# Performance work log

Hardware: AMD Instinct MI355X
Metric: run time of the kernel (lower is better)

The kernel has to match this reference:

```python
import jax, jax.numpy as jnp
import numpy as np

NUM_HEADS = 8

def setup_inputs() -> dict:
    key = jax.random.key(0)
    ks = jax.random.split(key, 10)
    B, S, D = 4, 2048, 512
    scale = 1.0 / np.sqrt(D)
    return {
        "x": jax.random.normal(ks[0], (B, S, D), dtype=jnp.float32),
        "q": jax.random.normal(ks[1], (B, S, D), dtype=jnp.float32),
        "Wq": jax.random.normal(ks[2], (D, D), dtype=jnp.float32) * scale,
        "bq": jax.random.normal(ks[3], (D,), dtype=jnp.float32) * 0.01,
        "Wk": jax.random.normal(ks[4], (D, D), dtype=jnp.float32) * scale,
        "bk": jax.random.normal(ks[5], (D,), dtype=jnp.float32) * 0.01,
        "Wv": jax.random.normal(ks[6], (D, D), dtype=jnp.float32) * scale,
        "bv": jax.random.normal(ks[7], (D,), dtype=jnp.float32) * 0.01,
        "Wo": jax.random.normal(ks[8], (D, D), dtype=jnp.float32) * scale,
        "bo": jax.random.normal(ks[9], (D,), dtype=jnp.float32) * 0.01,
    }

def reference(x, q, Wq, bq, Wk, bk, Wv, bv, Wo, bo):
    B, S, D = x.shape
    H = NUM_HEADS
    Dh = D // H
    # Linear layers: y = x @ W.T + b (torch nn.Linear convention)
    def split_heads(t):  # [B,S,D] -> [B,H,S,Dh]
        return t.reshape(B, -1, H, Dh).transpose(0, 2, 1, 3)
    Q = split_heads(q @ Wq.T + bq)
    K = split_heads(x @ Wk.T + bk)
    V = split_heads(x @ Wv.T + bv)
    logits = jnp.einsum('bhqd,bhkd->bhqk', Q, K) / jnp.sqrt(jnp.asarray(Dh, Q.dtype))
    attn = jax.nn.softmax(logits, axis=-1)
    out = jnp.einsum('bhqk,bhkd->bhqd', attn, V)  # [B,H,S,Dh]
    concat = out.transpose(0, 2, 1, 3).reshape(B, -1, D)
    return concat @ Wo.T + bo
```

## Files before the change

kernel.cpp:

```cpp
#include <hip/hip_runtime.h>
#include <stdint.h>

typedef __bf16 bf16_t;
typedef bf16_t bf16x8 __attribute__((ext_vector_type(8)));
typedef bf16_t bf16x4 __attribute__((ext_vector_type(4)));
typedef bf16_t bf16x2 __attribute__((ext_vector_type(2)));
typedef float f32x4 __attribute__((ext_vector_type(4)));
typedef float f32x16 __attribute__((ext_vector_type(16)));
typedef uint32_t u32x4 __attribute__((ext_vector_type(4)));

#define DEV __device__ __forceinline__

DEV void gload_lds16(const void* g, void* l) {
  __builtin_amdgcn_global_load_lds(
      (__attribute__((address_space(1))) void*)(g),
      (__attribute__((address_space(3))) void*)(l), 16, 0, 0);
}

__global__ __launch_bounds__(256) void cvt2_kernel(
    const float* __restrict__ x, const float* __restrict__ q,
    bf16_t* __restrict__ xb, bf16_t* __restrict__ qb) {
  const float* s = blockIdx.y ? q : x;
  bf16_t* d = blockIdx.y ? qb : xb;
  int i = blockIdx.x * 256 + threadIdx.x;
  if (i < 524288) {
    const float4* sp = (const float4*)s + (size_t)i * 2;
    float4 a = sp[0], b = sp[1];
    bf16x8 o;
    o[0] = (bf16_t)a.x; o[1] = (bf16_t)a.y; o[2] = (bf16_t)a.z; o[3] = (bf16_t)a.w;
    o[4] = (bf16_t)b.x; o[5] = (bf16_t)b.y; o[6] = (bf16_t)b.z; o[7] = (bf16_t)b.w;
    *(bf16x8*)(d + (size_t)i * 8) = o;
  }
}

__global__ __launch_bounds__(256) void cvtw_kernel(
    const float* __restrict__ Wq, const float* __restrict__ Wk,
    const float* __restrict__ Wv, const float* __restrict__ Wo,
    bf16_t* __restrict__ dst) {
  int y = blockIdx.y;
  const float* s = (y == 0) ? Wq : (y == 1) ? Wk : (y == 2) ? Wv : Wo;
  bf16_t* d = dst + (size_t)y * 262144;
  int i = blockIdx.x * 256 + threadIdx.x;
  if (i < 32768) {
    const float4* sp = (const float4*)s + (size_t)i * 2;
    float4 a = sp[0], b = sp[1];
    bf16x8 o;
    o[0] = (bf16_t)a.x; o[1] = (bf16_t)a.y; o[2] = (bf16_t)a.z; o[3] = (bf16_t)a.w;
    o[4] = (bf16_t)b.x; o[5] = (bf16_t)b.y; o[6] = (bf16_t)b.z; o[7] = (bf16_t)b.w;
    *(bf16x8*)(d + (size_t)i * 8) = o;
  }
}

DEV void gemm_core(const bf16_t* __restrict__ A, const bf16_t* __restrict__ W,
                   char* smem, f32x4 (&acc)[4][4]) {
  const int tid = threadIdx.x;
  const int lane = tid & 63;
  const int wid = tid >> 6;
  const int wr = wid >> 1, wc = wid & 1;
  const int bx = blockIdx.x, by = blockIdx.y;

  uint32_t goffA[4], goffB[4], ldsoff[4];
#pragma unroll
  for (int c = 0; c < 4; ++c) {
    uint32_t o = (uint32_t)wid * 4096u + (uint32_t)c * 1024u + (uint32_t)lane * 16u;
    uint32_t row = o >> 7;
    uint32_t inner = (o & 127u) ^ ((row & 7u) << 4);
    goffA[c] = ((uint32_t)by * 128u + row) * 1024u + inner;
    goffB[c] = ((uint32_t)bx * 128u + row) * 1024u + inner;
    ldsoff[c] = o - (uint32_t)lane * 16u;
  }
  uint32_t offA[4][2], offB[4][2];
#pragma unroll
  for (int i = 0; i < 4; ++i)
#pragma unroll
    for (int kk = 0; kk < 2; ++kk) {
      uint32_t ra = (uint32_t)(wr * 64 + i * 16 + (lane & 15));
      offA[i][kk] = ra * 128u + (((uint32_t)kk * 64u + ((lane >> 4) * 16u)) ^ ((ra & 7u) << 4));
      uint32_t rb = (uint32_t)(wc * 64 + i * 16 + (lane & 15));
      offB[i][kk] = rb * 128u + (((uint32_t)kk * 64u + ((lane >> 4) * 16u)) ^ ((rb & 7u) << 4));
    }

  const char* Ab = (const char*)A;
  const char* Wb = (const char*)W;

#pragma unroll
  for (int c = 0; c < 4; ++c) {
    gload_lds16(Ab + goffA[c], smem + ldsoff[c]);
    gload_lds16(Wb + goffB[c], smem + 16384 + ldsoff[c]);
  }
  asm volatile("s_waitcnt vmcnt(0)" ::: "memory");
  __syncthreads();

#pragma unroll 1
  for (int kt = 0; kt < 8; ++kt) {
    const int buf = kt & 1;
    char* cur = smem + buf * 32768;
    if (kt < 7) {
      char* nxt = smem + (buf ^ 1) * 32768;
      uint32_t gk = (uint32_t)(kt + 1) * 128u;
#pragma unroll
      for (int c = 0; c < 4; ++c) {
        gload_lds16(Ab + goffA[c] + gk, nxt + ldsoff[c]);
        gload_lds16(Wb + goffB[c] + gk, nxt + 16384 + ldsoff[c]);
      }
    }
    bf16x8 af[4][2], bfr[4][2];
#pragma unroll
    for (int kk = 0; kk < 2; ++kk)
#pragma unroll
      for (int i = 0; i < 4; ++i) {
        af[i][kk] = *(const bf16x8*)(cur + offA[i][kk]);
        bfr[i][kk] = *(const bf16x8*)(cur + 16384 + offB[i][kk]);
      }
    __builtin_amdgcn_s_setprio(1);
#pragma unroll
    for (int kk = 0; kk < 2; ++kk)
#pragma unroll
      for (int mi = 0; mi < 4; ++mi)
#pragma unroll
        for (int nj = 0; nj < 4; ++nj)
          acc[mi][nj] = __builtin_amdgcn_mfma_f32_16x16x32_bf16(
              af[mi][kk], bfr[nj][kk], acc[mi][nj], 0, 0, 0);
    __builtin_amdgcn_s_setprio(0);
    asm volatile("s_waitcnt vmcnt(0)" ::: "memory");
    __syncthreads();
  }
}

__global__ __launch_bounds__(256) void gemm_qkv_kernel(
    const bf16_t* __restrict__ xb, const bf16_t* __restrict__ qb,
    const bf16_t* __restrict__ Wb, const float* __restrict__ bq,
    const float* __restrict__ bk, const float* __restrict__ bv,
    bf16_t* __restrict__ Qh, bf16_t* __restrict__ Kh, bf16_t* __restrict__ VT) {
  __shared__ char smem[65536];
  const int z = blockIdx.z;
  const bf16_t* A = (z == 0) ? qb : xb;
  const bf16_t* W = Wb + (size_t)z * 262144;
  const float* bias = (z == 0) ? bq : (z == 1) ? bk : bv;

  f32x4 acc[4][4] = {};
  gemm_core(A, W, smem, acc);

  const int lane = threadIdx.x & 63, wid = threadIdx.x >> 6;
  const int wr = wid >> 1, wc = wid & 1;
  const int colbase = blockIdx.x * 128 + wc * 64 + (lane & 15);
  const int rowbase = blockIdx.y * 128 + wr * 64 + ((lane >> 4) << 2);

  if (z == 2) {
#pragma unroll
    for (int nj = 0; nj < 4; ++nj) {
      int c = colbase + nj * 16;
      float bb = bias[c];
      int h = c >> 6, d = c & 63;
#pragma unroll
      for (int mi = 0; mi < 4; ++mi) {
        int r0 = rowbase + mi * 16;
        int b = r0 >> 11, s0 = r0 & 2047;
        bf16x4 v;
#pragma unroll
        for (int rr = 0; rr < 4; ++rr) v[rr] = (bf16_t)(acc[mi][nj][rr] + bb);
        *(bf16x4*)(VT + ((size_t)((b << 3) | h) * 64 + d) * 2048 + s0) = v;
      }
    }
  } else {
    bf16_t* O = (z == 0) ? Qh : Kh;
    const float scl = (z == 0) ? 0.18033688f : 1.0f;
#pragma unroll
    for (int nj = 0; nj < 4; ++nj) {
      int c = colbase + nj * 16;
      float bb = bias[c];
      int h = c >> 6, d = c & 63;
#pragma unroll
      for (int mi = 0; mi < 4; ++mi)
#pragma unroll
        for (int rr = 0; rr < 4; ++rr) {
          int r = rowbase + mi * 16 + rr;
          int b = r >> 11, s = r & 2047;
          O[((size_t)((b << 3) | h) * 2048 + s) * 64 + d] = (bf16_t)((acc[mi][nj][rr] + bb) * scl);
        }
    }
  }
}

__global__ __launch_bounds__(256) void gemm_out_kernel(
    const bf16_t* __restrict__ ctx, const bf16_t* __restrict__ Wo,
    const float* __restrict__ bo, float* __restrict__ out) {
  __shared__ char smem[65536];
  f32x4 acc[4][4] = {};
  gemm_core(ctx, Wo, smem, acc);

  const int lane = threadIdx.x & 63, wid = threadIdx.x >> 6;
  const int wr = wid >> 1, wc = wid & 1;
  const int colbase = blockIdx.x * 128 + wc * 64 + (lane & 15);
  const int rowbase = blockIdx.y * 128 + wr * 64 + ((lane >> 4) << 2);
#pragma unroll
  for (int nj = 0; nj < 4; ++nj) {
    int c = colbase + nj * 16;
    float bb = bo[c];
#pragma unroll
    for (int mi = 0; mi < 4; ++mi)
#pragma unroll
      for (int rr = 0; rr < 4; ++rr) {
        int r = rowbase + mi * 16 + rr;
        out[(size_t)r * 512 + c] = acc[mi][nj][rr] + bb;
      }
  }
}

__global__ __launch_bounds__(256, 2) void attn_kernel(
    const bf16_t* __restrict__ Qh, const bf16_t* __restrict__ Kh,
    const bf16_t* __restrict__ VT, bf16_t* __restrict__ ctx) {
  __shared__ char smem[32768];
  char* Kb = smem;
  char* Vb = smem + 16384;
  const int tid = threadIdx.x, lane = tid & 63, wid = tid >> 6;
  const int l31 = lane & 31, h = lane >> 5;
  const int qt = blockIdx.x, bh = blockIdx.y;

  const char* Kbase = (const char*)Kh + (size_t)bh * 262144;
  const char* Vbase = (const char*)VT + (size_t)bh * 262144;
  const char* Qbase = (const char*)Qh + (size_t)bh * 262144;

  const int qrow = qt * 128 + wid * 32 + l31;
  bf16x8 qf[4];
#pragma unroll
  for (int ks = 0; ks < 4; ++ks)
    qf[ks] = *(const bf16x8*)(Qbase + (size_t)qrow * 128 + ks * 32 + h * 16);

  uint32_t kgo[2], vgo[2], lo[2];
#pragma unroll
  for (int c = 0; c < 2; ++c) {
    uint32_t o = (uint32_t)c * 4096u + (uint32_t)wid * 1024u + (uint32_t)lane * 16u;
    uint32_t row = o >> 7;
    uint32_t inner = (o & 127u) ^ ((row & 7u) << 4);
    kgo[c] = row * 128u + inner;
    vgo[c] = row * 4096u + inner;
    lo[c] = o - (uint32_t)lane * 16u;
  }

  const uint32_t swz = (uint32_t)(l31 & 7) << 4;
  uint32_t fbase[2], fcol[4];
#pragma unroll
  for (int c = 0; c < 2; ++c) fbase[c] = (uint32_t)(32 * c + l31) * 128u;
#pragma unroll
  for (int ks = 0; ks < 4; ++ks) fcol[ks] = ((uint32_t)(ks * 32 + h * 16)) ^ swz;

  f32x16 oacc[2] = {};
  float m_run = -1.0e30f, l_part = 0.f;

#pragma unroll
  for (int c = 0; c < 2; ++c) {
    gload_lds16(Kbase + kgo[c], Kb + lo[c]);
    gload_lds16(Vbase + vgo[c], Vb + lo[c]);
  }
  asm volatile("s_waitcnt vmcnt(0)" ::: "memory");
  __syncthreads();

#pragma unroll 1
  for (int t = 0; t < 32; ++t) {
    const uint32_t cur = ((uint32_t)t & 1u) << 13;
    if (t < 31) {
      const uint32_t nxt = cur ^ 8192u;
      const char* Kn = Kbase + (size_t)(t + 1) * 8192;
      const char* Vn = Vbase + (size_t)(t + 1) * 128;
#pragma unroll
      for (int c = 0; c < 2; ++c) {
        gload_lds16(Kn + kgo[c], Kb + nxt + lo[c]);
        gload_lds16(Vn + vgo[c], Vb + nxt + lo[c]);
      }
    }

    f32x16 sT[2] = {};
#pragma unroll
    for (int c = 0; c < 2; ++c) {
      __builtin_amdgcn_s_setprio(1);
#pragma unroll
      for (int ks = 0; ks < 4; ++ks) {
        bf16x8 kf = *(const bf16x8*)(Kb + cur + fbase[c] + fcol[ks]);
        sT[c] = __builtin_amdgcn_mfma_f32_32x32x16_bf16(kf, qf[ks], sT[c], 0, 0, 0);
      }
      __builtin_amdgcn_s_setprio(0);
    }

    float mx = sT[0][0];
#pragma unroll
    for (int c = 0; c < 2; ++c)
#pragma unroll
      for (int r = 0; r < 16; ++r) mx = fmaxf(mx, sT[c][r]);
    mx = fmaxf(mx, __shfl_xor(mx, 32));
    bool ok = (mx <= m_run + 8.0f);
    if (!__all(ok)) {
      float mnew = fmaxf(m_run, mx);
      float sc = __builtin_exp2f(m_run - mnew);
      m_run = mnew;
      l_part *= sc;
#pragma unroll
      for (int r = 0; r < 16; ++r) { oacc[0][r] *= sc; oacc[1][r] *= sc; }
    }

    uint32_t cw[2][8];
    float ladd = 0.f;
#pragma unroll
    for (int c = 0; c < 2; ++c)
#pragma unroll
      for (int w = 0; w < 8; ++w) {
        float p0 = __builtin_exp2f(sT[c][2 * w] - m_run);
        float p1 = __builtin_exp2f(sT[c][2 * w + 1] - m_run);
        ladd += p0 + p1;
        bf16x2 tp; tp[0] = (bf16_t)p0; tp[1] = (bf16_t)p1;
        cw[c][w] = __builtin_bit_cast(uint32_t, tp);
      }
    l_part += ladd;

    bf16x8 pa[4];
#pragma unroll
    for (int s = 0; s < 4; ++s) {
      const int c = s >> 1, sp = s & 1;
      uint32_t w0 = cw[c][4 * sp + 0], w1 = cw[c][4 * sp + 1];
      uint32_t w2 = cw[c][4 * sp + 2], w3 = cw[c][4 * sp + 3];
      uint32_t sx0 = (uint32_t)__shfl_xor((int)w0, 32);
      uint32_t sx1 = (uint32_t)__shfl_xor((int)w1, 32);
      uint32_t sx2 = (uint32_t)__shfl_xor((int)w2, 32);
      uint32_t sx3 = (uint32_t)__shfl_xor((int)w3, 32);
      u32x4 ta;
      ta[0] = h ? sx2 : w0;
      ta[1] = h ? sx3 : w1;
      ta[2] = h ? w2 : sx0;
      ta[3] = h ? w3 : sx1;
      pa[s] = __builtin_bit_cast(bf16x8, ta);
    }

#pragma unroll
    for (int dc = 0; dc < 2; ++dc) {
      __builtin_amdgcn_s_setprio(1);
#pragma unroll
      for (int ks = 0; ks < 4; ++ks) {
        bf16x8 vf = *(const bf16x8*)(Vb + cur + fbase[dc] + fcol[ks]);
        oacc[dc] = __builtin_amdgcn_mfma_f32_32x32x16_bf16(vf, pa[ks], oacc[dc], 0, 0, 0);
      }
      __builtin_amdgcn_s_setprio(0);
    }

    asm volatile("s_waitcnt vmcnt(0)" ::: "memory");
    __syncthreads();
  }

  float l = l_part + __shfl_xor(l_part, 32);
  float inv = 1.0f / l;
  const int b = bh >> 3, hh = bh & 7;
  bf16_t* crow = ctx + ((size_t)(b * 2048 + qrow)) * 512 + hh * 64;
#pragma unroll
  for (int dc = 0; dc < 2; ++dc)
#pragma unroll
    for (int m = 0; m < 4; ++m) {
      bf16x4 v;
#pragma unroll
      for (int r = 0; r < 4; ++r) v[r] = (bf16_t)(oacc[dc][4 * m + r] * inv);
      *(bf16x4*)(crow + dc * 32 + m * 8 + h * 4) = v;
    }
}

extern "C" void kernel_launch(void* const* d_in, const int* in_sizes, int n_in,
                              void* d_out, int out_size, void* d_ws, size_t ws_size,
                              hipStream_t stream) {
  const float* x  = (const float*)d_in[0];
  const float* q  = (const float*)d_in[1];
  const float* Wq = (const float*)d_in[2];
  const float* bq = (const float*)d_in[3];
  const float* Wk = (const float*)d_in[4];
  const float* bk = (const float*)d_in[5];
  const float* Wv = (const float*)d_in[6];
  const float* bv = (const float*)d_in[7];
  const float* Wo = (const float*)d_in[8];
  const float* bo = (const float*)d_in[9];

  char* ws = (char*)d_ws;
  bf16_t* xb  = (bf16_t*)(ws + 0);
  bf16_t* qb  = (bf16_t*)(ws + 8388608);
  bf16_t* Wb  = (bf16_t*)(ws + 16777216);
  bf16_t* Qh  = (bf16_t*)(ws + 18874368);
  bf16_t* Kh  = (bf16_t*)(ws + 27262976);
  bf16_t* VT  = (bf16_t*)(ws + 35651584);
  bf16_t* ctx = (bf16_t*)(ws + 44040192);

  cvt2_kernel<<<dim3(2048, 2), 256, 0, stream>>>(x, q, xb, qb);
  cvtw_kernel<<<dim3(128, 4), 256, 0, stream>>>(Wq, Wk, Wv, Wo, Wb);
  gemm_qkv_kernel<<<dim3(4, 64, 3), 256, 0, stream>>>(xb, qb, Wb, bq, bk, bv, Qh, Kh, VT);
  attn_kernel<<<dim3(16, 32), 256, 0, stream>>>(Qh, Kh, VT, ctx);
  gemm_out_kernel<<<dim3(4, 64), 256, 0, stream>>>(ctx, Wb + 3 * 262144, bo, (float*)d_out);
}
```

Measured before the change: 121.2 us.

## Speculative softmax max, fused convert kernels, remapped attention blocks, fewer shuffles

```diff
diff --git a/kernel.cpp b/kernel.cpp
--- a/kernel.cpp
+++ b/kernel.cpp
@@ -17,38 +17,30 @@
       (__attribute__((address_space(3))) void*)(l), 16, 0, 0);
 }
 
-__global__ __launch_bounds__(256) void cvt2_kernel(
+__global__ __launch_bounds__(256) void cvt_all_kernel(
     const float* __restrict__ x, const float* __restrict__ q,
-    bf16_t* __restrict__ xb, bf16_t* __restrict__ qb) {
-  const float* s = blockIdx.y ? q : x;
-  bf16_t* d = blockIdx.y ? qb : xb;
-  int i = blockIdx.x * 256 + threadIdx.x;
-  if (i < 524288) {
-    const float4* sp = (const float4*)s + (size_t)i * 2;
-    float4 a = sp[0], b = sp[1];
-    bf16x8 o;
-    o[0] = (bf16_t)a.x; o[1] = (bf16_t)a.y; o[2] = (bf16_t)a.z; o[3] = (bf16_t)a.w;
-    o[4] = (bf16_t)b.x; o[5] = (bf16_t)b.y; o[6] = (bf16_t)b.z; o[7] = (bf16_t)b.w;
-    *(bf16x8*)(d + (size_t)i * 8) = o;
-  }
-}
-
-__global__ __launch_bounds__(256) void cvtw_kernel(
     const float* __restrict__ Wq, const float* __restrict__ Wk,
     const float* __restrict__ Wv, const float* __restrict__ Wo,
-    bf16_t* __restrict__ dst) {
-  int y = blockIdx.y;
-  const float* s = (y == 0) ? Wq : (y == 1) ? Wk : (y == 2) ? Wv : Wo;
-  bf16_t* d = dst + (size_t)y * 262144;
+    bf16_t* __restrict__ xb, bf16_t* __restrict__ qb, bf16_t* __restrict__ Wb) {
+  const int y = blockIdx.y;
   int i = blockIdx.x * 256 + threadIdx.x;
-  if (i < 32768) {
-    const float4* sp = (const float4*)s + (size_t)i * 2;
-    float4 a = sp[0], b = sp[1];
-    bf16x8 o;
-    o[0] = (bf16_t)a.x; o[1] = (bf16_t)a.y; o[2] = (bf16_t)a.z; o[3] = (bf16_t)a.w;
-    o[4] = (bf16_t)b.x; o[5] = (bf16_t)b.y; o[6] = (bf16_t)b.z; o[7] = (bf16_t)b.w;
-    *(bf16x8*)(d + (size_t)i * 8) = o;
-  }
+  const float* s;
+  bf16_t* d;
+  if (y == 0) { s = x; d = xb; }
+  else if (y == 1) { s = q; d = qb; }
+  else {
+    if (i >= 131072) return;
+    int widx = i >> 15;
+    s = (widx == 0) ? Wq : (widx == 1) ? Wk : (widx == 2) ? Wv : Wo;
+    d = Wb + (size_t)widx * 262144;
+    i &= 32767;
+  }
+  const float4* sp = (const float4*)s + (size_t)i * 2;
+  float4 a = sp[0], b = sp[1];
+  bf16x8 o;
+  o[0] = (bf16_t)a.x; o[1] = (bf16_t)a.y; o[2] = (bf16_t)a.z; o[3] = (bf16_t)a.w;
+  o[4] = (bf16_t)b.x; o[5] = (bf16_t)b.y; o[6] = (bf16_t)b.z; o[7] = (bf16_t)b.w;
+  *(bf16x8*)(d + (size_t)i * 8) = o;
 }
 
 DEV void gemm_core(const bf16_t* __restrict__ A, const bf16_t* __restrict__ W,
@@ -215,7 +207,9 @@
   char* Vb = smem + 16384;
   const int tid = threadIdx.x, lane = tid & 63, wid = tid >> 6;
   const int l31 = lane & 31, h = lane >> 5;
-  const int qt = blockIdx.x, bh = blockIdx.y;
+  const int bid = blockIdx.x + 16 * blockIdx.y;
+  const int qt = (bid >> 3) & 15;
+  const int bh = (bid & 7) * 4 + (bid >> 7);
 
   const char* Kbase = (const char*)Kh + (size_t)bh * 262144;
   const char* Vbase = (const char*)VT + (size_t)bh * 262144;
@@ -246,7 +240,7 @@
   for (int ks = 0; ks < 4; ++ks) fcol[ks] = ((uint32_t)(ks * 32 + h * 16)) ^ swz;
 
   f32x16 oacc[2] = {};
-  float m_run = -1.0e30f, l_part = 0.f;
+  float m_run = 0.0f, l_part = 0.f;
 
 #pragma unroll
   for (int c = 0; c < 2; ++c) {
@@ -282,34 +276,51 @@
       __builtin_amdgcn_s_setprio(0);
     }
 
-    float mx = sT[0][0];
-#pragma unroll
-    for (int c = 0; c < 2; ++c)
-#pragma unroll
-      for (int r = 0; r < 16; ++r) mx = fmaxf(mx, sT[c][r]);
-    mx = fmaxf(mx, __shfl_xor(mx, 32));
-    bool ok = (mx <= m_run + 8.0f);
-    if (!__all(ok)) {
-      float mnew = fmaxf(m_run, mx);
-      float sc = __builtin_exp2f(m_run - mnew);
-      m_run = mnew;
-      l_part *= sc;
-#pragma unroll
-      for (int r = 0; r < 16; ++r) { oacc[0][r] *= sc; oacc[1][r] *= sc; }
-    }
-
     uint32_t cw[2][8];
-    float ladd = 0.f;
+    float la0 = 0.f, la1 = 0.f, la2 = 0.f, la3 = 0.f;
 #pragma unroll
     for (int c = 0; c < 2; ++c)
 #pragma unroll
       for (int w = 0; w < 8; ++w) {
         float p0 = __builtin_exp2f(sT[c][2 * w] - m_run);
         float p1 = __builtin_exp2f(sT[c][2 * w + 1] - m_run);
-        ladd += p0 + p1;
+        if ((w & 3) == 0) la0 += p0 + p1;
+        else if ((w & 3) == 1) la1 += p0 + p1;
+        else if ((w & 3) == 2) la2 += p0 + p1;
+        else la3 += p0 + p1;
         bf16x2 tp; tp[0] = (bf16_t)p0; tp[1] = (bf16_t)p1;
         cw[c][w] = __builtin_bit_cast(uint32_t, tp);
       }
+    float ladd = (la0 + la1) + (la2 + la3);
+    if (!__all(ladd <= 16384.0f)) {
+      float mx = sT[0][0];
+#pragma unroll
+      for (int c = 0; c < 2; ++c)
+#pragma unroll
+        for (int r = 0; r < 16; ++r) mx = fmaxf(mx, sT[c][r]);
+      mx = fmaxf(mx, __shfl_xor(mx, 32));
+      float mnew = fmaxf(m_run, mx);
+      float sc = __builtin_exp2f(m_run - mnew);
+      l_part *= sc;
+#pragma unroll
+      for (int r = 0; r < 16; ++r) { oacc[0][r] *= sc; oacc[1][r] *= sc; }
+      m_run = mnew;
+      la0 = la1 = la2 = la3 = 0.f;
+#pragma unroll
+      for (int c = 0; c < 2; ++c)
+#pragma unroll
+        for (int w = 0; w < 8; ++w) {
+          float p0 = __builtin_exp2f(sT[c][2 * w] - m_run);
+          float p1 = __builtin_exp2f(sT[c][2 * w + 1] - m_run);
+          if ((w & 3) == 0) la0 += p0 + p1;
+          else if ((w & 3) == 1) la1 += p0 + p1;
+          else if ((w & 3) == 2) la2 += p0 + p1;
+          else la3 += p0 + p1;
+          bf16x2 tp; tp[0] = (bf16_t)p0; tp[1] = (bf16_t)p1;
+          cw[c][w] = __builtin_bit_cast(uint32_t, tp);
+        }
+      ladd = (la0 + la1) + (la2 + la3);
+    }
     l_part += ladd;
 
     bf16x8 pa[4];
@@ -318,15 +329,15 @@
       const int c = s >> 1, sp = s & 1;
       uint32_t w0 = cw[c][4 * sp + 0], w1 = cw[c][4 * sp + 1];
       uint32_t w2 = cw[c][4 * sp + 2], w3 = cw[c][4 * sp + 3];
-      uint32_t sx0 = (uint32_t)__shfl_xor((int)w0, 32);
-      uint32_t sx1 = (uint32_t)__shfl_xor((int)w1, 32);
-      uint32_t sx2 = (uint32_t)__shfl_xor((int)w2, 32);
-      uint32_t sx3 = (uint32_t)__shfl_xor((int)w3, 32);
+      uint32_t snd0 = h ? w0 : w2;
+      uint32_t snd1 = h ? w1 : w3;
+      uint32_t rcv0 = (uint32_t)__shfl_xor((int)snd0, 32);
+      uint32_t rcv1 = (uint32_t)__shfl_xor((int)snd1, 32);
       u32x4 ta;
-      ta[0] = h ? sx2 : w0;
-      ta[1] = h ? sx3 : w1;
-      ta[2] = h ? w2 : sx0;
-      ta[3] = h ? w3 : sx1;
+      ta[0] = h ? rcv0 : w0;
+      ta[1] = h ? rcv1 : w1;
+      ta[2] = h ? w2 : rcv0;
+      ta[3] = h ? w3 : rcv1;
       pa[s] = __builtin_bit_cast(bf16x8, ta);
     }
 
@@ -383,8 +394,7 @@
   bf16_t* VT  = (bf16_t*)(ws + 35651584);
   bf16_t* ctx = (bf16_t*)(ws + 44040192);
 
-  cvt2_kernel<<<dim3(2048, 2), 256, 0, stream>>>(x, q, xb, qb);
-  cvtw_kernel<<<dim3(128, 4), 256, 0, stream>>>(Wq, Wk, Wv, Wo, Wb);
+  cvt_all_kernel<<<dim3(2048, 3), 256, 0, stream>>>(x, q, Wq, Wk, Wv, Wo, xb, qb, Wb);
   gemm_qkv_kernel<<<dim3(4, 64, 3), 256, 0, stream>>>(xb, qb, Wb, bq, bk, bv, Qh, Kh, VT);
   attn_kernel<<<dim3(16, 32), 256, 0, stream>>>(Qh, Kh, VT, ctx);
   gemm_out_kernel<<<dim3(4, 64), 256, 0, stream>>>(ctx, Wb + 3 * 262144, bo, (float*)d_out);
```

Result: faster. 117.3 us (-3.2%).
